# Performance work log

Measured on AMD Instinct MI355X. Metric: run time of the kernel, lower is better.

## Reference

```python
import jax, jax.numpy as jnp
import numpy as np

N_NODES = 50000
N_EDGES = 800000
IN_CH = 8
CH = 128
EATTR = 6
N_BBOX = 2000
N_CLASSES = 32
N_BLOCKS = 3  # head + 2 residual blocks; n_blocks_out = 3
FUSION = CH * N_BLOCKS  # 384


def _kaiming(key, shape):
    fan_in = shape[0]
    return jax.random.normal(key, shape, dtype=jnp.float32) * np.sqrt(2.0 / fan_in)


def setup_inputs() -> dict:
    key = jax.random.key(0)
    ks = jax.random.split(key, 24)
    x = jax.random.normal(ks[0], (N_NODES, IN_CH), dtype=jnp.float32)
    e_attr = jax.random.normal(ks[1], (N_EDGES, EATTR), dtype=jnp.float32)
    edge = jax.random.randint(ks[2], (2, N_EDGES), 0, N_NODES, dtype=jnp.int32)
    bbox_idx = jnp.sort(jax.random.randint(ks[3], (N_NODES,), 0, N_BBOX, dtype=jnp.int32))
    d_head = 2 * IN_CH + EATTR   # 22
    d_blk = 2 * CH + EATTR       # 262
    inp = {
        "x": x, "e_attr": e_attr,
        "W_h": _kaiming(ks[4], (d_head, CH)), "b_h": jnp.zeros((CH,), jnp.float32),
        "Ws_h": _kaiming(ks[5], (d_head, CH)), "bs_h": jnp.zeros((CH,), jnp.float32),
        "Wb": jnp.stack([_kaiming(ks[6], (d_blk, CH)), _kaiming(ks[7], (d_blk, CH))]),
        "bb": jnp.zeros((2, CH), jnp.float32),
        "Wbs": jnp.stack([_kaiming(ks[8], (d_blk, CH)), _kaiming(ks[9], (d_blk, CH))]),
        "bbs": jnp.zeros((2, CH), jnp.float32),
        "W_f": _kaiming(ks[10], (FUSION, 1024)), "b_f": jnp.zeros((1024,), jnp.float32),
        "W_fs": _kaiming(ks[11], (FUSION, 1024)), "b_fs": jnp.zeros((1024,), jnp.float32),
        "W1": _kaiming(ks[12], ((FUSION + 1024) * 2, 512)), "b1": jnp.zeros((512,), jnp.float32),
        "W2": _kaiming(ks[13], (512, 256)), "b2": jnp.zeros((256,), jnp.float32),
        "W3": _kaiming(ks[14], (256, N_CLASSES)), "b3": jnp.zeros((N_CLASSES,), jnp.float32),
        "edge": edge, "bbox_idx": bbox_idx,
    }
    return inp


def _seg_max0(h, idx, n):
    m = jax.ops.segment_max(h, idx, num_segments=n)
    return jnp.where(jnp.isneginf(m), 0.0, m)  # empty segments -> 0 (torch_scatter semantics)


def _seg_mean(h, idx, n):
    s = jax.ops.segment_sum(h, idx, num_segments=n)
    c = jax.ops.segment_sum(jnp.ones((h.shape[0], 1), h.dtype), idx, num_segments=n)
    return s / jnp.maximum(c, 1.0)


def _graph_conv(x, x_node, src, dst, e_attr, W, b, Ws, bs, n):
    # edge message: MLP(concat(x_i, x_j - x_i, e_attr)); max-scatter for node stream,
    # mean-scatter for super stream (gp2 = two global-pool reductions)
    h = jax.nn.relu(jnp.concatenate([x[src], x[dst] - x[src], e_attr], axis=1) @ W + b)
    f = _seg_max0(h, dst, n)
    hs = jax.nn.relu(jnp.concatenate([x_node[src], x_node[dst] - x_node[src], e_attr], axis=1) @ Ws + bs)
    f_super = _seg_mean(hs, dst, n)
    return f, f_super


def reference(x, e_attr, W_h, b_h, Ws_h, bs_h, Wb, bb, Wbs, bbs,
              W_f, b_f, W_fs, b_fs, W1, b1, W2, b2, W3, b3, edge, bbox_idx):
    src, dst = edge[0], edge[1]
    n = x.shape[0]
    # head conv
    f, fs = _graph_conv(x, x, src, dst, e_attr, W_h, b_h, Ws_h, bs_h, n)
    feats, feats_super = [f], [fs]
    # residual blocks
    for i in range(N_BLOCKS - 1):
        g, gs = _graph_conv(feats[-1], feats_super[-1], src, dst, e_attr,
                            Wb[i], bb[i], Wbs[i], bbs[i], n)
        feats.append(g + feats[-1])
        feats_super.append(gs + feats_super[-1])
    feats = jnp.concatenate(feats, axis=1)              # [N, 384]
    fusion = jax.nn.relu(feats @ W_f + b_f)             # [N, 1024]
    out_feat = jnp.concatenate([fusion, feats], axis=1) # [N, 1408]
    feats_super = jnp.concatenate(feats_super, axis=1)  # [N, 384]
    feats_super = _seg_mean(feats_super, bbox_idx, N_BBOX)            # [B, 384]
    fusion_super = jax.nn.relu(feats_super @ W_fs + b_fs)             # [B, 1024]
    out_super = jnp.concatenate([fusion_super, feats_super], axis=1)  # [B, 1408]
    pooled = _seg_max0(out_feat, bbox_idx, N_BBOX)                    # [B, 1408]
    h = jnp.concatenate([pooled, out_super], axis=1)                  # [B, 2816]
    h = jax.nn.relu(h @ W1 + b1)
    h = jax.nn.relu(h @ W2 + b2)  # dropout=0 / eval mode
    logits = h @ W3 + b3          # classifier == 'softmax': raw logits returned
    return logits
```

## Files before the change

kernel.cpp:

```cpp
#include <hip/hip_runtime.h>
#include <stdint.h>

#define NN      50000
#define NE      800000
#define INCH    8
#define CH      128
#define EA      6
#define NB      2000
#define NB_PAD  2048
#define NCLS    32
#define FUS     384
#define K1      2816
#define SCAN_NBLK 49

typedef _Float16 half8 __attribute__((ext_vector_type(8)));
typedef _Float16 h2 __attribute__((ext_vector_type(2)));
typedef float f32x4 __attribute__((ext_vector_type(4)));

__global__ __launch_bounds__(256) void k_deg(const int* __restrict__ edge,
                                             int* __restrict__ deg) {
  int e = blockIdx.x * 256 + threadIdx.x;
  if (e < NE) atomicAdd(&deg[edge[NE + e]], 1);
}

__global__ __launch_bounds__(1024) void k_scan1(const int* __restrict__ deg,
                                                int* __restrict__ row_ptr,
                                                int* __restrict__ bsum) {
  __shared__ int wsum[16];
  const int t = threadIdx.x, lane = t & 63, w = t >> 6;
  const int i = blockIdx.x * 1024 + t;
  int x = (i < NN) ? deg[i] : 0;
#pragma unroll
  for (int off = 1; off < 64; off <<= 1) {
    int y = __shfl_up(x, off, 64);
    if (lane >= off) x += y;
  }
  if (lane == 63) wsum[w] = x;
  __syncthreads();
  if (w == 0 && lane < 16) {
    int s = wsum[lane];
#pragma unroll
    for (int off = 1; off < 16; off <<= 1) {
      int y = __shfl_up(s, off, 64);
      if (lane >= off) s += y;
    }
    wsum[lane] = s;
  }
  __syncthreads();
  int incl = x + ((w == 0) ? 0 : wsum[w - 1]);
  if (i < NN) row_ptr[i + 1] = incl;
  if (t == 1023) bsum[blockIdx.x] = incl;
}

__global__ __launch_bounds__(64) void k_scan2(int* __restrict__ bsum) {
  const int t = threadIdx.x;
  int x = (t < SCAN_NBLK) ? bsum[t] : 0;
#pragma unroll
  for (int off = 1; off < 64; off <<= 1) {
    int y = __shfl_up(x, off, 64);
    if (t >= off) x += y;
  }
  int ex = __shfl_up(x, 1, 64);
  if (t == 0) ex = 0;
  if (t < SCAN_NBLK) bsum[t] = ex;
}

__global__ __launch_bounds__(256) void k_scan3(const int* __restrict__ bsum,
                                               int* __restrict__ row_ptr) {
  const int i = blockIdx.x * 256 + threadIdx.x;
  if (i == 0) row_ptr[0] = 0;
  if (i < NN) row_ptr[i + 1] += bsum[i >> 10];
}

__global__ __launch_bounds__(256) void k_fill(
    const int* __restrict__ edge, const float* __restrict__ eattr,
    const int* __restrict__ row_ptr, int* __restrict__ cursor,
    int* __restrict__ ssrc, _Float16* __restrict__ sea8) {
  int e = blockIdx.x * 256 + threadIdx.x;
  if (e >= NE) return;
  int s = edge[e], d = edge[NE + e];
  int idx = row_ptr[d] + atomicAdd(&cursor[d], 1);
  ssrc[idx] = s;
  half8 v;
#pragma unroll
  for (int j = 0; j < EA; ++j) v[j] = (_Float16)eattr[(size_t)e * EA + j];
  v[6] = (_Float16)0.f; v[7] = (_Float16)0.f;
  *(half8*)(sea8 + (size_t)idx * 8) = v;
}

__global__ __launch_bounds__(256) void k_segstart(const int* __restrict__ bbox,
                                                  int* __restrict__ seg) {
  int i = blockIdx.x * 256 + threadIdx.x;
  if (i >= NN) return;
  int bc = bbox[i];
  int bp = (i == 0) ? -1 : bbox[i - 1];
  for (int j = bp + 1; j <= bc; ++j) seg[j] = i;
  if (i == NN - 1)
    for (int j = bc + 1; j <= NB; ++j) seg[j] = NN;
}

__global__ __launch_bounds__(256) void k_node_pq(
    const float* __restrict__ X, int ldx, int K,
    const float* __restrict__ WN, const float* __restrict__ bN,
    const float* __restrict__ WS, const float* __restrict__ bS,
    _Float16* __restrict__ PQi, _Float16* __restrict__ Qi) {
  const int sel = blockIdx.y;
  const float* W = sel ? WS : WN;
  const float* bias = sel ? bS : bN;
  const int t = threadIdx.x, lane = t & 63, wv = t >> 6;
  const int nbase = blockIdx.x * 32 + wv * 8;
  const int c = lane * 2;
  const float2 bv = *(const float2*)(bias + c);
  float2 pacc[8], qacc[8];
#pragma unroll
  for (int u = 0; u < 8; ++u) { pacc[u] = bv; qacc[u] = make_float2(0.f, 0.f); }
  const int xrow = min(nbase + (lane >> 3), NN - 1);
  const int xk = lane & 7;
  for (int k0 = 0; k0 < K; k0 += 8) {
    const float xv = X[(size_t)xrow * ldx + k0 + xk];
#pragma unroll
    for (int j = 0; j < 8; ++j) {
      const float2 w1 = *(const float2*)(W + (size_t)(k0 + j) * CH + c);
      const float2 w2 = *(const float2*)(W + (size_t)(K + k0 + j) * CH + c);
      const float2 wd = {w1.x - w2.x, w1.y - w2.y};
#pragma unroll
      for (int u = 0; u < 8; ++u) {
        const float xs = __shfl(xv, u * 8 + j, 64);
        pacc[u].x += xs * wd.x; pacc[u].y += xs * wd.y;
        qacc[u].x += xs * w2.x; qacc[u].y += xs * w2.y;
      }
    }
  }
#pragma unroll
  for (int u = 0; u < 8; ++u) {
    const int node = nbase + u;
    if (node < NN) {
      const size_t o = ((size_t)node * 64 + lane) * 4 + sel * 2;
      *(h2*)(PQi + o) = (h2){(_Float16)pacc[u].x, (_Float16)pacc[u].y};
      *(h2*)(Qi + o)  = (h2){(_Float16)qacc[u].x, (_Float16)qacc[u].y};
    }
  }
}

__global__ __launch_bounds__(64) void k_cvtWnpq(
    const float* __restrict__ WbAll, const float* __restrict__ WbsAll,
    _Float16* __restrict__ whN, _Float16* __restrict__ whS) {
  const int blk = blockIdx.z;
  const float* W = (blockIdx.y ? WbsAll : WbAll) + (size_t)blk * 262 * CH;
  _Float16* wh   = (blockIdx.y ? whS : whN) + (size_t)blk * 32768;
  const int c = blockIdx.x >> 4, tile = blockIdx.x & 15;
  const int L = threadIdx.x;
  const int n = tile * 16 + (L & 15);
  const int k0 = c * 32 + (L >> 4) * 8;
  half8 v;
#pragma unroll
  for (int j = 0; j < 8; ++j) {
    const int k = k0 + j;
    float val;
    if (n < CH) val = W[(size_t)k * CH + n] - W[(size_t)(CH + k) * CH + n];
    else        val = W[(size_t)(CH + k) * CH + (n - CH)];
    v[j] = (_Float16)val;
  }
  *(half8*)(wh + (((size_t)(c * 16 + tile)) * 64 + L) * 8) = v;
}

__global__ __launch_bounds__(256) void k_npq_mfma(
    const float* __restrict__ Xn, const float* __restrict__ Xs, int ldx,
    const _Float16* __restrict__ whN, const _Float16* __restrict__ whS,
    const float* __restrict__ biasN, const float* __restrict__ biasS,
    _Float16* __restrict__ PQi, _Float16* __restrict__ Qi) {
  const int sel = blockIdx.y;
  const float* X = sel ? Xs : Xn;
  const _Float16* wh = sel ? whS : whN;
  const float* bias = sel ? biasS : biasN;
  const int t = threadIdx.x, lane = t & 63, wv = t >> 6;
  const int nbase = blockIdx.x * 64;
  const int m = lane & 15, quad = lane >> 4;
  f32x4 acc[4][4];
#pragma unroll
  for (int i = 0; i < 4; ++i)
#pragma unroll
    for (int nt = 0; nt < 4; ++nt) acc[i][nt] = (f32x4){0.f, 0.f, 0.f, 0.f};
#pragma unroll
  for (int ks = 0; ks < 4; ++ks) {
    half8 b[4];
#pragma unroll
    for (int nt = 0; nt < 4; ++nt)
      b[nt] = *(const half8*)(wh + (((size_t)(ks * 16 + wv * 4 + nt)) * 64 + lane) * 8);
#pragma unroll
    for (int i = 0; i < 4; ++i) {
      const int row = min(nbase + i * 16 + m, NN - 1);
      const float* src = X + (size_t)row * ldx + ks * 32 + quad * 8;
      const float4 f0 = *(const float4*)src;
      const float4 f1 = *(const float4*)(src + 4);
      half8 a;
      a[0] = (_Float16)f0.x; a[1] = (_Float16)f0.y;
      a[2] = (_Float16)f0.z; a[3] = (_Float16)f0.w;
      a[4] = (_Float16)f1.x; a[5] = (_Float16)f1.y;
      a[6] = (_Float16)f1.z; a[7] = (_Float16)f1.w;
#pragma unroll
      for (int nt = 0; nt < 4; ++nt)
        acc[i][nt] = __builtin_amdgcn_mfma_f32_16x16x32_f16(a, b[nt], acc[i][nt],
                                                            0, 0, 0);
    }
  }
#pragma unroll
  for (int i = 0; i < 4; ++i)
#pragma unroll
    for (int nt = 0; nt < 4; ++nt) {
      const int col = wv * 64 + nt * 16 + m;
      const float bv = (col < CH) ? bias[col] : 0.f;
#pragma unroll
      for (int r = 0; r < 4; ++r) {
        const int row = nbase + i * 16 + quad * 4 + r;
        if (row < NN) {
          const float v = acc[i][nt][r] + bv;
          if (col < CH)
            PQi[((size_t)row * 64 + (col >> 1)) * 4 + sel * 2 + (col & 1)] =
                (_Float16)v;
          else {
            const int qc = col - CH;
            Qi[((size_t)row * 64 + (qc >> 1)) * 4 + sel * 2 + (qc & 1)] =
                (_Float16)v;
          }
        }
      }
    }
}

__global__ __launch_bounds__(256) void k_conv2(
    const int* __restrict__ row_ptr, const int* __restrict__ ssrc,
    const _Float16* __restrict__ sea8,
    const _Float16* __restrict__ PQi, const _Float16* __restrict__ Qi,
    const float* __restrict__ Cn, const float* __restrict__ Cs,
    float* __restrict__ feats, float* __restrict__ sfeats,
    int cur, int prev) {
  const int t = threadIdx.x;
  const int lane = t & 63;
  const int node = blockIdx.x * 4 + (t >> 6);
  const int c = lane * 2;
  h2 cwnh[EA], cwsh[EA];
#pragma unroll
  for (int j = 0; j < EA; ++j) {
    const float2 a = *(const float2*)(Cn + j * CH + c);
    const float2 b = *(const float2*)(Cs + j * CH + c);
    cwnh[j] = (h2){(_Float16)a.x, (_Float16)a.y};
    cwsh[j] = (h2){(_Float16)b.x, (_Float16)b.y};
  }
  int i0 = __builtin_amdgcn_readfirstlane(row_ptr[node]);
  int i1 = __builtin_amdgcn_readfirstlane(row_ptr[node + 1]);
  const uint2 qv = *(const uint2*)(Qi + ((size_t)node * 64 + lane) * 4);
  const h2 qnh = *(const h2*)&qv.x;
  const h2 qsh = *(const h2*)&qv.y;
  const _Float16* pqL = PQi + (size_t)lane * 4;
  h2 anh = (h2){(_Float16)0.f, (_Float16)0.f};
  float as0 = 0.f, as1 = 0.f;
  const h2 zero = (h2){(_Float16)0.f, (_Float16)0.f};
#define COMP(PV, J)                                                        \
  {                                                                        \
    unsigned w0 = __shfl((int)ea_l.x, (J), 64);                            \
    unsigned w1 = __shfl((int)ea_l.y, (J), 64);                            \
    unsigned w2 = __shfl((int)ea_l.z, (J), 64);                            \
    const h2 ea01 = *(const h2*)&w0;                                       \
    const h2 ea23 = *(const h2*)&w1;                                       \
    const h2 ea45 = *(const h2*)&w2;                                       \
    h2 vn = *(const h2*)&PV.x + qnh;                                       \
    h2 vs = *(const h2*)&PV.y + qsh;                                       \
    h2 b;                                                                  \
    b = (h2){ea01[0], ea01[0]}; vn += b * cwnh[0]; vs += b * cwsh[0];      \
    b = (h2){ea01[1], ea01[1]}; vn += b * cwnh[1]; vs += b * cwsh[1];      \
    b = (h2){ea23[0], ea23[0]}; vn += b * cwnh[2]; vs += b * cwsh[2];      \
    b = (h2){ea23[1], ea23[1]}; vn += b * cwnh[3]; vs += b * cwsh[3];      \
    b = (h2){ea45[0], ea45[0]}; vn += b * cwnh[4]; vs += b * cwsh[4];      \
    b = (h2){ea45[1], ea45[1]}; vn += b * cwnh[5]; vs += b * cwsh[5];      \
    anh = __builtin_elementwise_max(anh, vn);                              \
    const h2 vsr = __builtin_elementwise_max(vs, zero);                    \
    as0 += (float)vsr[0]; as1 += (float)vsr[1];                            \
  }
  for (int base = i0; base < i1; base += 64) {
    const int cnt = min(64, i1 - base);
    int s_l = 0;
    uint4 ea_l = {0u, 0u, 0u, 0u};
    if (lane < cnt) {
      s_l = ssrc[base + lane];
      ea_l = *(const uint4*)(sea8 + (size_t)(base + lane) * 8);
    }
    int j = 0;
    for (; j + 4 <= cnt; j += 4) {
      const int sa = __shfl(s_l, j, 64);
      const int sb = __shfl(s_l, j + 1, 64);
      const int sc = __shfl(s_l, j + 2, 64);
      const int sd = __shfl(s_l, j + 3, 64);
      const uint2 pva = *(const uint2*)(pqL + (size_t)sa * 256);
      const uint2 pvb = *(const uint2*)(pqL + (size_t)sb * 256);
      const uint2 pvc = *(const uint2*)(pqL + (size_t)sc * 256);
      const uint2 pvd = *(const uint2*)(pqL + (size_t)sd * 256);
      COMP(pva, j) COMP(pvb, j + 1) COMP(pvc, j + 2) COMP(pvd, j + 3)
    }
    for (; j < cnt; ++j) {
      const int sa = __shfl(s_l, j, 64);
      const uint2 pva = *(const uint2*)(pqL + (size_t)sa * 256);
      COMP(pva, j)
    }
  }
#undef COMP
  float an0 = (float)anh[0], an1 = (float)anh[1];
  const float inv = 1.f / fmaxf((float)(i1 - i0), 1.f);
  as0 *= inv; as1 *= inv;
  const size_t o = (size_t)node * FUS + (size_t)cur * CH + c;
  if (prev >= 0) {
    const size_t op = (size_t)node * FUS + (size_t)prev * CH + c;
    const float2 prn = *(const float2*)(feats + op);
    const float2 prs = *(const float2*)(sfeats + op);
    an0 += prn.x; an1 += prn.y;
    as0 += prs.x; as1 += prs.y;
  }
  float2 on = {an0, an1}, os = {as0, as1};
  *(float2*)(feats + o) = on;
  *(float2*)(sfeats + o) = os;
}

__global__ __launch_bounds__(64) void k_cvtApack(const float* __restrict__ feats,
                                                 _Float16* __restrict__ ap) {
  const int rb = blockIdx.x / 12, ks = blockIdx.x % 12;
  const int L = threadIdx.x, m = L & 15, quad = L >> 4;
#pragma unroll
  for (int i = 0; i < 4; ++i) {
    const int row = rb * 64 + i * 16 + m;
    const int rowc = min(row, NN - 1);
    const float* src = feats + (size_t)rowc * FUS + ks * 32 + quad * 8;
    half8 v;
    if (row < NN) {
      const float4 f0 = *(const float4*)src;
      const float4 f1 = *(const float4*)(src + 4);
      v[0] = (_Float16)f0.x; v[1] = (_Float16)f0.y;
      v[2] = (_Float16)f0.z; v[3] = (_Float16)f0.w;
      v[4] = (_Float16)f1.x; v[5] = (_Float16)f1.y;
      v[6] = (_Float16)f1.z; v[7] = (_Float16)f1.w;
    } else {
#pragma unroll
      for (int j = 0; j < 8; ++j) v[j] = (_Float16)0.f;
    }
    *(half8*)(ap + (((size_t)(rb * 12 + ks) * 4 + i) * 64 + L) * 8) = v;
  }
}

template <int N, int NT>
__global__ __launch_bounds__(64) void k_cvtB(const float* __restrict__ W,
                                             _Float16* __restrict__ wh) {
  const int c = blockIdx.x / NT;
  const int tile = blockIdx.x % NT;
  const int L = threadIdx.x;
  const int n = tile * 16 + (L & 15);
  const int k0 = c * 32 + (L >> 4) * 8;
  half8 v;
#pragma unroll
  for (int j = 0; j < 8; ++j) v[j] = (_Float16)W[(size_t)(k0 + j) * N + n];
  *(half8*)(wh + (((size_t)(c * NT + tile)) * 64 + L) * 8) = v;
}

__global__ __launch_bounds__(256, 6) void k_pool_mfma(
    const _Float16* __restrict__ aP, const _Float16* __restrict__ wh,
    const int* __restrict__ bbox, const float* __restrict__ bf,
    float* __restrict__ pooled) {
  __shared__ float cl[32 * 132];
  __shared__ int s_bb[64];
  _Float16* abuf = (_Float16*)cl;
  const int t = threadIdx.x, lane = t & 63, wv = t >> 6;
  const int fid = blockIdx.x;
  const int xcd = fid & 7, slot = fid >> 3;
  const int cg = slot & 7;
  const int rb = xcd * 98 + (slot >> 3);
  const int nbase = rb * 64;
  const int m = lane & 15, quad = lane >> 4;
  if (t < 64) s_bb[t] = bbox[min(nbase + t, NN - 1)];
  f32x4 acc[4][2];
#pragma unroll
  for (int i = 0; i < 4; ++i)
#pragma unroll
    for (int nt = 0; nt < 2; ++nt) acc[i][nt] = (f32x4){0.f, 0.f, 0.f, 0.f};
  const _Float16* apc = aP + (size_t)rb * 12 * 2048 + (size_t)wv * 512 +
                        (size_t)lane * 8;
  const _Float16* bp = wh + ((size_t)(cg * 8 + wv * 2) * 64 + lane) * 8;
  _Float16* wslot = abuf + wv * 512 + lane * 8;
  const _Float16* rbase = abuf + lane * 8;
  half8 b0 = *(const half8*)(bp);
  half8 b1 = *(const half8*)(bp + 512);
  half8 rA = *(const half8*)(apc);
  *(half8*)(wslot) = rA;
  half8 rN = *(const half8*)(apc + 2048);
  __syncthreads();
#pragma unroll
  for (int ks = 0; ks < 12; ++ks) {
    const int cur = ks & 1;
    half8 nb0, nb1;
    if (ks < 11) {
      nb0 = *(const half8*)(bp + (size_t)(ks + 1) * 32768);
      nb1 = *(const half8*)(bp + (size_t)(ks + 1) * 32768 + 512);
    }
#pragma unroll
    for (int i = 0; i < 4; ++i) {
      const half8 a = *(const half8*)(rbase + cur * 2048 + i * 512);
      acc[i][0] = __builtin_amdgcn_mfma_f32_16x16x32_f16(a, b0, acc[i][0], 0, 0, 0);
      acc[i][1] = __builtin_amdgcn_mfma_f32_16x16x32_f16(a, b1, acc[i][1], 0, 0, 0);
    }
    if (ks < 11) {
      *(half8*)(wslot + (cur ^ 1) * 2048) = rN;
      b0 = nb0; b1 = nb1;
    }
    if (ks < 10) rN = *(const half8*)(apc + (size_t)(ks + 2) * 2048);
    __syncthreads();
  }
  const int col = t & 127, rh = t >> 7;
  const int gcol = cg * 128 + col;
  const float bias = bf[gcol];
#pragma unroll
  for (int p = 0; p < 2; ++p) {
    __syncthreads();
#pragma unroll
    for (int ii = 0; ii < 2; ++ii)
#pragma unroll
      for (int nt = 0; nt < 2; ++nt) {
        const int scol = wv * 32 + nt * 16 + m;
#pragma unroll
        for (int r = 0; r < 4; ++r)
          cl[(ii * 16 + quad * 4 + r) * 132 + scol] = acc[p * 2 + ii][nt][r];
      }
    __syncthreads();
    int curb = -1;
    float mx = 0.f;
    for (int rr = 0; rr < 16; ++rr) {
      const int rl = rh * 16 + rr;
      const int node = nbase + p * 32 + rl;
      if (node >= NN) break;
      const int bid = s_bb[p * 32 + rl];
      const float v = fmaxf(cl[rl * 132 + col] + bias, 0.f);
      if (bid != curb) {
        if (curb >= 0)
          atomicMax((unsigned*)(pooled + (size_t)curb * 1408 + gcol),
                    __float_as_uint(mx));
        curb = bid;
        mx = v;
      } else {
        mx = fmaxf(mx, v);
      }
    }
    if (curb >= 0)
      atomicMax((unsigned*)(pooled + (size_t)curb * 1408 + gcol),
                __float_as_uint(mx));
  }
}

__global__ __launch_bounds__(256) void k_poolraw(
    const float* __restrict__ feats, const float* __restrict__ sfeats,
    const int* __restrict__ seg, float* __restrict__ pooled,
    float* __restrict__ sb, _Float16* __restrict__ sbH) {
  const int b = blockIdx.x, t = threadIdx.x;
  if (t >= 192) return;
  const int c2 = t * 2;
  const int n0 = __builtin_amdgcn_readfirstlane(seg[b]);
  const int n1 = __builtin_amdgcn_readfirstlane(seg[b + 1]);
  float2 fmx = {0.f, 0.f}, ss = {0.f, 0.f};
  for (int n = n0; n < n1; ++n) {
    const float2 f2 = *(const float2*)(feats + (size_t)n * FUS + c2);
    fmx.x = fmaxf(fmx.x, f2.x); fmx.y = fmaxf(fmx.y, f2.y);
    const float2 s2 = *(const float2*)(sfeats + (size_t)n * FUS + c2);
    ss.x += s2.x; ss.y += s2.y;
  }
  *(float2*)(pooled + (size_t)b * 1408 + 1024 + c2) = fmx;
  const float inv = 1.f / fmaxf((float)(n1 - n0), 1.f);
  float2 o = {ss.x * inv, ss.y * inv};
  *(float2*)(sb + (size_t)b * FUS + c2) = o;
  *(h2*)(sbH + (size_t)b * FUS + c2) = (h2){(_Float16)o.x, (_Float16)o.y};
}

__global__ __launch_bounds__(256) void k_fsup_mfma(
    const _Float16* __restrict__ sbH, const _Float16* __restrict__ wh,
    const float* __restrict__ bfs, float* __restrict__ fs) {
  const int t = threadIdx.x, lane = t & 63, wv = t >> 6;
  const int nbase = blockIdx.x * 64;
  const int cg = blockIdx.y;
  const int m = lane & 15, quad = lane >> 4;
  f32x4 acc[4][2];
#pragma unroll
  for (int i = 0; i < 4; ++i)
#pragma unroll
    for (int nt = 0; nt < 2; ++nt) acc[i][nt] = (f32x4){0.f, 0.f, 0.f, 0.f};
  const _Float16* ap = sbH + (size_t)(nbase + m) * FUS + quad * 8;
  const _Float16* bp = wh + ((size_t)(cg * 8 + wv * 2) * 64 + lane) * 8;
#pragma unroll
  for (int ks = 0; ks < 12; ++ks) {
    const half8 b0 = *(const half8*)(bp + (size_t)ks * 32768);
    const half8 b1v = *(const half8*)(bp + (size_t)ks * 32768 + 512);
#pragma unroll
    for (int i = 0; i < 4; ++i) {
      const half8 a = *(const half8*)(ap + (size_t)(i * 16) * FUS + ks * 32);
      acc[i][0] = __builtin_amdgcn_mfma_f32_16x16x32_f16(a, b0, acc[i][0], 0, 0, 0);
      acc[i][1] = __builtin_amdgcn_mfma_f32_16x16x32_f16(a, b1v, acc[i][1], 0, 0, 0);
    }
  }
#pragma unroll
  for (int i = 0; i < 4; ++i)
#pragma unroll
    for (int nt = 0; nt < 2; ++nt) {
      const int gcol = cg * 128 + wv * 32 + nt * 16 + m;
      const float bias = bfs[gcol];
#pragma unroll
      for (int r = 0; r < 4; ++r) {
        const int row = nbase + i * 16 + quad * 4 + r;
        if (row < NB)
          fs[(size_t)row * 1024 + gcol] = fmaxf(acc[i][nt][r] + bias, 0.f);
      }
    }
}

__global__ __launch_bounds__(256) void k_cvt_cat(
    const float* __restrict__ pooled, const float* __restrict__ fsup,
    const float* __restrict__ sb, _Float16* __restrict__ bbH) {
  const size_t off = ((size_t)blockIdx.x * 256 + threadIdx.x) * 8;
  const int row = (int)(off / K1);
  const int col = (int)(off - (size_t)row * K1);
  half8 v;
  if (row < NB) {
    const float* src;
    if (col < 1408)      src = pooled + (size_t)row * 1408 + col;
    else if (col < 2432) src = fsup + (size_t)row * 1024 + (col - 1408);
    else                 src = sb + (size_t)row * FUS + (col - 2432);
    const float4 f0 = *(const float4*)src;
    const float4 f1 = *(const float4*)(src + 4);
    v[0] = (_Float16)f0.x; v[1] = (_Float16)f0.y;
    v[2] = (_Float16)f0.z; v[3] = (_Float16)f0.w;
    v[4] = (_Float16)f1.x; v[5] = (_Float16)f1.y;
    v[6] = (_Float16)f1.z; v[7] = (_Float16)f1.w;
  } else {
#pragma unroll
    for (int j = 0; j < 8; ++j) v[j] = (_Float16)0.f;
  }
  *(half8*)(bbH + off) = v;
}

__global__ __launch_bounds__(256) void k_mlp1_mfma(
    const _Float16* __restrict__ bbH, const _Float16* __restrict__ wh,
    const float* __restrict__ b1, float* __restrict__ h1) {
  const int t = threadIdx.x, lane = t & 63, wv = t >> 6;
  const int nbase = blockIdx.x * 64;
  const int cg = blockIdx.y;
  const int m = lane & 15, quad = lane >> 4;
  f32x4 acc[4][2];
#pragma unroll
  for (int i = 0; i < 4; ++i)
#pragma unroll
    for (int nt = 0; nt < 2; ++nt) acc[i][nt] = (f32x4){0.f, 0.f, 0.f, 0.f};
  const _Float16* ap = bbH + (size_t)(nbase + m) * K1 + quad * 8;
  const _Float16* bp = wh + ((size_t)(cg * 8 + wv * 2) * 64 + lane) * 8;
#pragma unroll 4
  for (int ks = 0; ks < 88; ++ks) {
    const half8 b0 = *(const half8*)(bp + (size_t)ks * 16384);
    const half8 b1v = *(const half8*)(bp + (size_t)ks * 16384 + 512);
#pragma unroll
    for (int i = 0; i < 4; ++i) {
      const half8 a = *(const half8*)(ap + (size_t)(i * 16) * K1 + ks * 32);
      acc[i][0] = __builtin_amdgcn_mfma_f32_16x16x32_f16(a, b0, acc[i][0], 0, 0, 0);
      acc[i][1] = __builtin_amdgcn_mfma_f32_16x16x32_f16(a, b1v, acc[i][1], 0, 0, 0);
    }
  }
#pragma unroll
  for (int i = 0; i < 4; ++i)
#pragma unroll
    for (int nt = 0; nt < 2; ++nt) {
      const int gcol = cg * 128 + wv * 32 + nt * 16 + m;
      const float bias = b1[gcol];
#pragma unroll
      for (int r = 0; r < 4; ++r) {
        const int row = nbase + i * 16 + quad * 4 + r;
        if (row < NB)
          h1[(size_t)row * 512 + gcol] = fmaxf(acc[i][nt][r] + bias, 0.f);
      }
    }
}

__global__ __launch_bounds__(256) void k_mlp2(
    const float* __restrict__ h1, const float* __restrict__ W2,
    const float* __restrict__ b2, float* __restrict__ h2o) {
  const int r0 = blockIdx.x * 8, t = threadIdx.x;
  float acc[8];
#pragma unroll
  for (int u = 0; u < 8; ++u) acc[u] = 0.f;
  for (int k = 0; k < 512; ++k) {
    float w = W2[(size_t)k * 256 + t];
#pragma unroll
    for (int u = 0; u < 8; ++u) acc[u] += h1[(size_t)(r0 + u) * 512 + k] * w;
  }
  float bv = b2[t];
#pragma unroll
  for (int u = 0; u < 8; ++u)
    h2o[(size_t)(r0 + u) * 256 + t] = fmaxf(acc[u] + bv, 0.f);
}

__global__ __launch_bounds__(256) void k_mlp3(
    const float* __restrict__ h2i, const float* __restrict__ W3,
    const float* __restrict__ b3, float* __restrict__ out) {
  const int r0 = blockIdx.x * 8, t = threadIdx.x;
  const int u = t >> 5, oc = t & 31;
  const float* x = h2i + (size_t)(r0 + u) * 256;
  float acc = 0.f;
  for (int k = 0; k < 256; ++k) acc += x[k] * W3[(size_t)k * 32 + oc];
  out[(size_t)(r0 + u) * 32 + oc] = acc + b3[oc];
}

extern "C" void kernel_launch(void* const* d_in, const int* in_sizes, int n_in,
                              void* d_out, int out_size, void* d_ws, size_t ws_size,
                              hipStream_t stream) {
  const float* x     = (const float*)d_in[0];
  const float* eattr = (const float*)d_in[1];
  const float* W_h   = (const float*)d_in[2];
  const float* b_h   = (const float*)d_in[3];
  const float* Ws_h  = (const float*)d_in[4];
  const float* bs_h  = (const float*)d_in[5];
  const float* Wb    = (const float*)d_in[6];
  const float* bb    = (const float*)d_in[7];
  const float* Wbs   = (const float*)d_in[8];
  const float* bbs   = (const float*)d_in[9];
  const float* W_f   = (const float*)d_in[10];
  const float* b_f   = (const float*)d_in[11];
  const float* W_fs  = (const float*)d_in[12];
  const float* b_fs  = (const float*)d_in[13];
  const float* W1    = (const float*)d_in[14];
  const float* b1    = (const float*)d_in[15];
  const float* W2    = (const float*)d_in[16];
  const float* b2    = (const float*)d_in[17];
  const float* W3    = (const float*)d_in[18];
  const float* b3    = (const float*)d_in[19];
  const int*   edge  = (const int*)d_in[20];
  const int*   bbox  = (const int*)d_in[21];
  float* out = (float*)d_out;

  float* p = (float*)d_ws;
  float* feats  = p; p += (size_t)NN * FUS;
  float* sfeats = p; p += (size_t)NN * FUS;
  float* PQ     = p; p += (size_t)2 * NN * CH;
  _Float16* PQi = (_Float16*)PQ;
  _Float16* Qi  = PQi + (size_t)NN * 256;
  _Float16* aPack = (_Float16*)PQ;
  _Float16* WfH   = aPack + (size_t)784 * 12 * 2048;
  float* pooled   = (float*)(WfH + (size_t)FUS * 1024);
  float* sb   = PQ;
  float* fsup = sb + (size_t)NB * FUS;
  float* h1   = fsup + (size_t)NB * 1024;
  float* h2b  = h1 + (size_t)NB * 512;
  _Float16* bbH = (_Float16*)(h2b + (size_t)NB * 256);
  _Float16* W1H = bbH + (size_t)NB_PAD * K1;
  _Float16* sea8 = (_Float16*)p;
  int* ssrc    = (int*)(sea8 + (size_t)NE * 8);
  int* row_ptr = ssrc + NE;
  int* deg     = row_ptr + NN + 1;
  int* cursor  = deg + NN;
  int* seg     = cursor + NN;
  _Float16* WcatN = (_Float16*)(seg + NB + 1);
  _Float16* WcatS = WcatN + (size_t)2 * 128 * 256;
  int* bsum = (int*)(WcatS + (size_t)2 * 128 * 256);
  _Float16* sbH = (_Float16*)(((uintptr_t)(bsum + SCAN_NBLK) + 127) &
                              ~(uintptr_t)127);
  _Float16* WfsH = sbH + (size_t)NB_PAD * FUS;

  hipMemsetAsync(deg, 0, 2 * NN * sizeof(int), stream);

  k_deg<<<(NE + 255) / 256, 256, 0, stream>>>(edge, deg);
  k_scan1<<<SCAN_NBLK, 1024, 0, stream>>>(deg, row_ptr, bsum);
  k_scan2<<<1, 64, 0, stream>>>(bsum);
  k_scan3<<<(NN + 255) / 256, 256, 0, stream>>>(bsum, row_ptr);
  k_fill<<<(NE + 255) / 256, 256, 0, stream>>>(edge, eattr, row_ptr, cursor,
                                               ssrc, sea8);
  k_segstart<<<(NN + 255) / 256, 256, 0, stream>>>(bbox, seg);

  const int npq_grid = (NN + 31) / 32;

  k_node_pq<<<dim3(npq_grid, 2), 256, 0, stream>>>(x, INCH, INCH, W_h, b_h,
                                                   Ws_h, bs_h, PQi, Qi);
  k_conv2<<<NN / 4, 256, 0, stream>>>(row_ptr, ssrc, sea8, PQi, Qi,
                                      W_h + 2 * INCH * CH, Ws_h + 2 * INCH * CH,
                                      feats, sfeats, 0, -1);

  k_cvtWnpq<<<dim3(64, 2, 2), 64, 0, stream>>>(Wb, Wbs, WcatN, WcatS);
  for (int i = 0; i < 2; ++i) {
    const float* Wi  = Wb  + (size_t)i * 262 * CH;
    const float* bi  = bb  + (size_t)i * CH;
    const float* Wsi = Wbs + (size_t)i * 262 * CH;
    const float* bsi = bbs + (size_t)i * CH;
    k_npq_mfma<<<dim3((NN + 63) / 64, 2), 256, 0, stream>>>(
        feats + i * CH, sfeats + i * CH, FUS, WcatN + (size_t)i * 32768,
        WcatS + (size_t)i * 32768, bi, bsi, PQi, Qi);
    k_conv2<<<NN / 4, 256, 0, stream>>>(row_ptr, ssrc, sea8, PQi, Qi,
                                        Wi + 2 * CH * CH, Wsi + 2 * CH * CH,
                                        feats, sfeats, i + 1, i);
  }

  k_cvtApack<<<784 * 12, 64, 0, stream>>>(feats, aPack);
  k_cvtB<1024, 64><<<12 * 64, 64, 0, stream>>>(W_f, WfH);
  k_cvtB<1024, 64><<<12 * 64, 64, 0, stream>>>(W_fs, WfsH);
  hipMemsetAsync(pooled, 0, (size_t)NB * 1408 * sizeof(float), stream);
  k_pool_mfma<<<784 * 8, 256, 0, stream>>>(aPack, WfH, bbox, b_f, pooled);
  k_poolraw<<<NB, 256, 0, stream>>>(feats, sfeats, seg, pooled, sb, sbH);
  k_fsup_mfma<<<dim3(NB_PAD / 64, 8), 256, 0, stream>>>(sbH, WfsH, b_fs, fsup);

  k_cvt_cat<<<(int)(((size_t)NB_PAD * K1 / 8) / 256), 256, 0, stream>>>(
      pooled, fsup, sb, bbH);
  k_cvtB<512, 32><<<88 * 32, 64, 0, stream>>>(W1, W1H);
  k_mlp1_mfma<<<dim3(NB_PAD / 64, 4), 256, 0, stream>>>(bbH, W1H, b1, h1);
  k_mlp2<<<NB / 8, 256, 0, stream>>>(h1, W2, b2, h2b);
  k_mlp3<<<NB / 8, 256, 0, stream>>>(h2b, W3, b3, out);
}
```

Baseline: 845.0 us.

## Store node features in fp16 and drop the A-pack conversion kernel

Node and super feature buffers change from fp32 to fp16, so the conv kernel writes half2, and the npq GEMM and pooling GEMM read fp16 rows directly. This removes the separate k_cvtApack pass and halves feature memory traffic in the conv, npq, poolraw and pooling kernels. Buffers are padded to a multiple of 64 rows and the pad is zeroed. The conv gather loop also gains an 8-way unrolled stage to keep more loads in flight. The cost is lower precision in the residual accumulation and in the pooled raw features, and the pooling GEMM now reads strided rows instead of a packed layout.

```diff
diff --git a/kernel.cpp b/kernel.cpp
--- a/kernel.cpp
+++ b/kernel.cpp
@@ -2,6 +2,7 @@
 #include <stdint.h>
 
 #define NN      50000
+#define NN_PAD  50176
 #define NE      800000
 #define INCH    8
 #define CH      128
@@ -165,12 +166,12 @@
 }
 
 __global__ __launch_bounds__(256) void k_npq_mfma(
-    const float* __restrict__ Xn, const float* __restrict__ Xs, int ldx,
+    const _Float16* __restrict__ Xn, const _Float16* __restrict__ Xs, int ldx,
     const _Float16* __restrict__ whN, const _Float16* __restrict__ whS,
     const float* __restrict__ biasN, const float* __restrict__ biasS,
     _Float16* __restrict__ PQi, _Float16* __restrict__ Qi) {
   const int sel = blockIdx.y;
-  const float* X = sel ? Xs : Xn;
+  const _Float16* X = sel ? Xs : Xn;
   const _Float16* wh = sel ? whS : whN;
   const float* bias = sel ? biasS : biasN;
   const int t = threadIdx.x, lane = t & 63, wv = t >> 6;
@@ -190,14 +191,7 @@
 #pragma unroll
     for (int i = 0; i < 4; ++i) {
       const int row = min(nbase + i * 16 + m, NN - 1);
-      const float* src = X + (size_t)row * ldx + ks * 32 + quad * 8;
-      const float4 f0 = *(const float4*)src;
-      const float4 f1 = *(const float4*)(src + 4);
-      half8 a;
-      a[0] = (_Float16)f0.x; a[1] = (_Float16)f0.y;
-      a[2] = (_Float16)f0.z; a[3] = (_Float16)f0.w;
-      a[4] = (_Float16)f1.x; a[5] = (_Float16)f1.y;
-      a[6] = (_Float16)f1.z; a[7] = (_Float16)f1.w;
+      const half8 a = *(const half8*)(X + (size_t)row * ldx + ks * 32 + quad * 8);
 #pragma unroll
       for (int nt = 0; nt < 4; ++nt)
         acc[i][nt] = __builtin_amdgcn_mfma_f32_16x16x32_f16(a, b[nt], acc[i][nt],
@@ -233,7 +227,7 @@
     const _Float16* __restrict__ sea8,
     const _Float16* __restrict__ PQi, const _Float16* __restrict__ Qi,
     const float* __restrict__ Cn, const float* __restrict__ Cs,
-    float* __restrict__ feats, float* __restrict__ sfeats,
+    _Float16* __restrict__ feats, _Float16* __restrict__ sfeats,
     int cur, int prev) {
   const int t = threadIdx.x;
   const int lane = t & 63;
@@ -286,21 +280,35 @@
       ea_l = *(const uint4*)(sea8 + (size_t)(base + lane) * 8);
     }
     int j = 0;
+    for (; j + 8 <= cnt; j += 8) {
+      const int s0 = __shfl(s_l, j, 64),     s1 = __shfl(s_l, j + 1, 64);
+      const int s2 = __shfl(s_l, j + 2, 64), s3 = __shfl(s_l, j + 3, 64);
+      const int s4 = __shfl(s_l, j + 4, 64), s5 = __shfl(s_l, j + 5, 64);
+      const int s6 = __shfl(s_l, j + 6, 64), s7 = __shfl(s_l, j + 7, 64);
+      const uint2 p0 = *(const uint2*)(pqL + (size_t)s0 * 256);
+      const uint2 p1 = *(const uint2*)(pqL + (size_t)s1 * 256);
+      const uint2 p2 = *(const uint2*)(pqL + (size_t)s2 * 256);
+      const uint2 p3 = *(const uint2*)(pqL + (size_t)s3 * 256);
+      const uint2 p4 = *(const uint2*)(pqL + (size_t)s4 * 256);
+      const uint2 p5 = *(const uint2*)(pqL + (size_t)s5 * 256);
+      const uint2 p6 = *(const uint2*)(pqL + (size_t)s6 * 256);
+      const uint2 p7 = *(const uint2*)(pqL + (size_t)s7 * 256);
+      COMP(p0, j)     COMP(p1, j + 1) COMP(p2, j + 2) COMP(p3, j + 3)
+      COMP(p4, j + 4) COMP(p5, j + 5) COMP(p6, j + 6) COMP(p7, j + 7)
+    }
     for (; j + 4 <= cnt; j += 4) {
-      const int sa = __shfl(s_l, j, 64);
-      const int sb = __shfl(s_l, j + 1, 64);
-      const int sc = __shfl(s_l, j + 2, 64);
-      const int sd = __shfl(s_l, j + 3, 64);
-      const uint2 pva = *(const uint2*)(pqL + (size_t)sa * 256);
-      const uint2 pvb = *(const uint2*)(pqL + (size_t)sb * 256);
-      const uint2 pvc = *(const uint2*)(pqL + (size_t)sc * 256);
-      const uint2 pvd = *(const uint2*)(pqL + (size_t)sd * 256);
-      COMP(pva, j) COMP(pvb, j + 1) COMP(pvc, j + 2) COMP(pvd, j + 3)
+      const int s0 = __shfl(s_l, j, 64),     s1 = __shfl(s_l, j + 1, 64);
+      const int s2 = __shfl(s_l, j + 2, 64), s3 = __shfl(s_l, j + 3, 64);
+      const uint2 p0 = *(const uint2*)(pqL + (size_t)s0 * 256);
+      const uint2 p1 = *(const uint2*)(pqL + (size_t)s1 * 256);
+      const uint2 p2 = *(const uint2*)(pqL + (size_t)s2 * 256);
+      const uint2 p3 = *(const uint2*)(pqL + (size_t)s3 * 256);
+      COMP(p0, j) COMP(p1, j + 1) COMP(p2, j + 2) COMP(p3, j + 3)
     }
     for (; j < cnt; ++j) {
-      const int sa = __shfl(s_l, j, 64);
-      const uint2 pva = *(const uint2*)(pqL + (size_t)sa * 256);
-      COMP(pva, j)
+      const int s0 = __shfl(s_l, j, 64);
+      const uint2 p0 = *(const uint2*)(pqL + (size_t)s0 * 256);
+      COMP(p0, j)
     }
   }
 #undef COMP
@@ -310,39 +318,13 @@
   const size_t o = (size_t)node * FUS + (size_t)cur * CH + c;
   if (prev >= 0) {
     const size_t op = (size_t)node * FUS + (size_t)prev * CH + c;
-    const float2 prn = *(const float2*)(feats + op);
-    const float2 prs = *(const float2*)(sfeats + op);
-    an0 += prn.x; an1 += prn.y;
-    as0 += prs.x; as1 += prs.y;
-  }
-  float2 on = {an0, an1}, os = {as0, as1};
-  *(float2*)(feats + o) = on;
-  *(float2*)(sfeats + o) = os;
-}
-
-__global__ __launch_bounds__(64) void k_cvtApack(const float* __restrict__ feats,
-                                                 _Float16* __restrict__ ap) {
-  const int rb = blockIdx.x / 12, ks = blockIdx.x % 12;
-  const int L = threadIdx.x, m = L & 15, quad = L >> 4;
-#pragma unroll
-  for (int i = 0; i < 4; ++i) {
-    const int row = rb * 64 + i * 16 + m;
-    const int rowc = min(row, NN - 1);
-    const float* src = feats + (size_t)rowc * FUS + ks * 32 + quad * 8;
-    half8 v;
-    if (row < NN) {
-      const float4 f0 = *(const float4*)src;
-      const float4 f1 = *(const float4*)(src + 4);
-      v[0] = (_Float16)f0.x; v[1] = (_Float16)f0.y;
-      v[2] = (_Float16)f0.z; v[3] = (_Float16)f0.w;
-      v[4] = (_Float16)f1.x; v[5] = (_Float16)f1.y;
-      v[6] = (_Float16)f1.z; v[7] = (_Float16)f1.w;
-    } else {
-#pragma unroll
-      for (int j = 0; j < 8; ++j) v[j] = (_Float16)0.f;
-    }
-    *(half8*)(ap + (((size_t)(rb * 12 + ks) * 4 + i) * 64 + L) * 8) = v;
-  }
+    const h2 prn = *(const h2*)(feats + op);
+    const h2 prs = *(const h2*)(sfeats + op);
+    an0 += (float)prn[0]; an1 += (float)prn[1];
+    as0 += (float)prs[0]; as1 += (float)prs[1];
+  }
+  *(h2*)(feats + o)  = (h2){(_Float16)an0, (_Float16)an1};
+  *(h2*)(sfeats + o) = (h2){(_Float16)as0, (_Float16)as1};
 }
 
 template <int N, int NT>
@@ -360,7 +342,7 @@
 }
 
 __global__ __launch_bounds__(256, 6) void k_pool_mfma(
-    const _Float16* __restrict__ aP, const _Float16* __restrict__ wh,
+    const _Float16* __restrict__ feats16, const _Float16* __restrict__ wh,
     const int* __restrict__ bbox, const float* __restrict__ bf,
     float* __restrict__ pooled) {
   __shared__ float cl[32 * 132];
@@ -379,8 +361,7 @@
   for (int i = 0; i < 4; ++i)
 #pragma unroll
     for (int nt = 0; nt < 2; ++nt) acc[i][nt] = (f32x4){0.f, 0.f, 0.f, 0.f};
-  const _Float16* apc = aP + (size_t)rb * 12 * 2048 + (size_t)wv * 512 +
-                        (size_t)lane * 8;
+  const _Float16* apc = feats16 + (size_t)(nbase + wv * 16 + m) * FUS + quad * 8;
   const _Float16* bp = wh + ((size_t)(cg * 8 + wv * 2) * 64 + lane) * 8;
   _Float16* wslot = abuf + wv * 512 + lane * 8;
   const _Float16* rbase = abuf + lane * 8;
@@ -388,7 +369,7 @@
   half8 b1 = *(const half8*)(bp + 512);
   half8 rA = *(const half8*)(apc);
   *(half8*)(wslot) = rA;
-  half8 rN = *(const half8*)(apc + 2048);
+  half8 rN = *(const half8*)(apc + 32);
   __syncthreads();
 #pragma unroll
   for (int ks = 0; ks < 12; ++ks) {
@@ -408,7 +389,7 @@
       *(half8*)(wslot + (cur ^ 1) * 2048) = rN;
       b0 = nb0; b1 = nb1;
     }
-    if (ks < 10) rN = *(const half8*)(apc + (size_t)(ks + 2) * 2048);
+    if (ks < 10) rN = *(const half8*)(apc + (size_t)(ks + 2) * 32);
     __syncthreads();
   }
   const int col = t & 127, rh = t >> 7;
@@ -452,7 +433,7 @@
 }
 
 __global__ __launch_bounds__(256) void k_poolraw(
-    const float* __restrict__ feats, const float* __restrict__ sfeats,
+    const _Float16* __restrict__ feats, const _Float16* __restrict__ sfeats,
     const int* __restrict__ seg, float* __restrict__ pooled,
     float* __restrict__ sb, _Float16* __restrict__ sbH) {
   const int b = blockIdx.x, t = threadIdx.x;
@@ -462,10 +443,10 @@
   const int n1 = __builtin_amdgcn_readfirstlane(seg[b + 1]);
   float2 fmx = {0.f, 0.f}, ss = {0.f, 0.f};
   for (int n = n0; n < n1; ++n) {
-    const float2 f2 = *(const float2*)(feats + (size_t)n * FUS + c2);
-    fmx.x = fmaxf(fmx.x, f2.x); fmx.y = fmaxf(fmx.y, f2.y);
-    const float2 s2 = *(const float2*)(sfeats + (size_t)n * FUS + c2);
-    ss.x += s2.x; ss.y += s2.y;
+    const h2 f2 = *(const h2*)(feats + (size_t)n * FUS + c2);
+    fmx.x = fmaxf(fmx.x, (float)f2[0]); fmx.y = fmaxf(fmx.y, (float)f2[1]);
+    const h2 s2 = *(const h2*)(sfeats + (size_t)n * FUS + c2);
+    ss.x += (float)s2[0]; ss.y += (float)s2[1];
   }
   *(float2*)(pooled + (size_t)b * 1408 + 1024 + c2) = fmx;
   const float inv = 1.f / fmaxf((float)(n1 - n0), 1.f);
@@ -635,22 +616,20 @@
   const int*   bbox  = (const int*)d_in[21];
   float* out = (float*)d_out;
 
-  float* p = (float*)d_ws;
-  float* feats  = p; p += (size_t)NN * FUS;
-  float* sfeats = p; p += (size_t)NN * FUS;
-  float* PQ     = p; p += (size_t)2 * NN * CH;
+  _Float16* feats  = (_Float16*)d_ws;
+  _Float16* sfeats = feats + (size_t)NN_PAD * FUS;
+  float* PQ = (float*)(sfeats + (size_t)NN_PAD * FUS);
   _Float16* PQi = (_Float16*)PQ;
   _Float16* Qi  = PQi + (size_t)NN * 256;
-  _Float16* aPack = (_Float16*)PQ;
-  _Float16* WfH   = aPack + (size_t)784 * 12 * 2048;
-  float* pooled   = (float*)(WfH + (size_t)FUS * 1024);
   float* sb   = PQ;
   float* fsup = sb + (size_t)NB * FUS;
   float* h1   = fsup + (size_t)NB * 1024;
   float* h2b  = h1 + (size_t)NB * 512;
   _Float16* bbH = (_Float16*)(h2b + (size_t)NB * 256);
   _Float16* W1H = bbH + (size_t)NB_PAD * K1;
-  _Float16* sea8 = (_Float16*)p;
+  _Float16* WfH = (_Float16*)PQ + (size_t)784 * 12 * 2048;
+  float* pooled = (float*)(WfH + (size_t)FUS * 1024);
+  _Float16* sea8 = (_Float16*)(PQ + (size_t)2 * NN * CH);
   int* ssrc    = (int*)(sea8 + (size_t)NE * 8);
   int* row_ptr = ssrc + NE;
   int* deg     = row_ptr + NN + 1;
@@ -664,6 +643,8 @@
   _Float16* WfsH = sbH + (size_t)NB_PAD * FUS;
 
   hipMemsetAsync(deg, 0, 2 * NN * sizeof(int), stream);
+  hipMemsetAsync(feats + (size_t)NN * FUS, 0,
+                 (size_t)(NN_PAD - NN) * FUS * sizeof(_Float16), stream);
 
   k_deg<<<(NE + 255) / 256, 256, 0, stream>>>(edge, deg);
   k_scan1<<<SCAN_NBLK, 1024, 0, stream>>>(deg, row_ptr, bsum);
@@ -695,11 +676,10 @@
                                         feats, sfeats, i + 1, i);
   }
 
-  k_cvtApack<<<784 * 12, 64, 0, stream>>>(feats, aPack);
   k_cvtB<1024, 64><<<12 * 64, 64, 0, stream>>>(W_f, WfH);
   k_cvtB<1024, 64><<<12 * 64, 64, 0, stream>>>(W_fs, WfsH);
   hipMemsetAsync(pooled, 0, (size_t)NB * 1408 * sizeof(float), stream);
-  k_pool_mfma<<<784 * 8, 256, 0, stream>>>(aPack, WfH, bbox, b_f, pooled);
+  k_pool_mfma<<<784 * 8, 256, 0, stream>>>(feats, WfH, bbox, b_f, pooled);
   k_poolraw<<<NB, 256, 0, stream>>>(feats, sfeats, seg, pooled, sb, sbH);
   k_fsup_mfma<<<dim3(NB_PAD / 64, 8), 256, 0, stream>>>(sbH, WfsH, b_fs, fsup);
 
```

New measurement: 787.7 us. -6.8%, faster.
